# Kernel tuning notes

Hardware: AMD Instinct MI355X
Metric: run time of the kernel (lower is better)

## Reference

```python
import jax, jax.numpy as jnp
import numpy as np
from math import pi

RADIUS = 40.0  # radius_scale
B, N = 1, 512


def map_polar_sqr(x, y, eps=1e-9):
    r = jnp.sqrt(x * x + y * y + eps)
    cond1 = (x == 0.0) & (y == 0.0)
    cond2 = (jnp.abs(y) <= jnp.abs(x)) & (~cond1)
    sx = jnp.where(x == 0.0, 1.0, x)  # safe denominators
    sy = jnp.where(y == 0.0, 1.0, y)
    c = 4.0 / pi
    x2 = jnp.sign(x) * r
    y2 = c * jnp.sign(x) * r * jnp.arctan(y / sx)
    x3 = c * jnp.sign(y) * r * jnp.arctan(x / sy)
    y3 = jnp.sign(y) * r
    x_out = jnp.where(cond1, 0.0, jnp.where(cond2, x2, x3))
    y_out = jnp.where(cond1, 0.0, jnp.where(cond2, y2, y3))
    return x_out, y_out


def axis_weights(g, size):
    # F.grid_sample bilinear, align_corners=False, padding_mode='zeros':
    # pixel coord = ((g+1)*size - 1)/2; linear weights on floor/floor+1,
    # out-of-range taps drop to zero automatically (idx only covers 0..size-1).
    c = ((g + 1.0) * size - 1.0) * 0.5
    i0 = jnp.floor(c)
    f = c - i0
    idx = jnp.arange(size, dtype=g.dtype)
    m0 = (idx == i0[..., None]).astype(g.dtype)
    m1 = (idx == i0[..., None] + 1.0).astype(g.dtype)
    return (1.0 - f)[..., None] * m0 + f[..., None] * m1  # [..., size]


def cts_conv(kernel, field, center, feat, mask, radius):
    # kernel: [o, i, kD, kH, kW]; field/center: [b, n/m, 3]; feat: [b, n, i]; mask: [b, n, 1]
    rel = (field[:, None] - center[:, :, None]) / radius            # [b,m,n,3]
    r2 = jnp.sum(rel * rel, -1)                                     # [b,m,n]
    att = jax.nn.relu((1.0 - r2) ** 3)[..., None] * mask[:, None]   # [b,m,n,1]
    xs, ys = map_polar_sqr(rel[..., 0], rel[..., 1])
    zs = rel[..., 2]
    kD, kH, kW = kernel.shape[2:]
    # grid_sample coord order: grid x -> W (last dim), y -> H, z -> D (first spatial dim)
    wz = axis_weights(zs, kD)
    wy = axis_weights(ys, kH)
    wx = axis_weights(xs, kW)
    w = jnp.einsum('bmnz,bmny,bmnx->bmnzyx', wz, wy, wx)
    w = w.reshape(*w.shape[:3], -1)                                 # [b,m,n,g=kD*kH*kW]
    fa = feat[:, None] * att                                        # [b,m,n,i]
    # exact trilinear interp + neighbor contraction without the [b,m,n,o,i] tensor:
    t = jnp.einsum('bmng,bmni->bmgi', w, fa)                        # [b,m,g,i]
    K = kernel.reshape(kernel.shape[0], kernel.shape[1], -1)        # [o,i,g]
    return jnp.einsum('bmgi,oig->bmo', t, K)


def setup_inputs() -> dict:
    key = jax.random.key(0)
    ks = jax.random.split(key, 24)

    def kern(k, o, i):
        return (jax.random.uniform(k, (o, i, 4, 4, 4), dtype=jnp.float32) - 0.5) / float(np.sqrt(i))

    def lin(kw, kb, o, i):
        return (jax.random.normal(kw, (o, i), dtype=jnp.float32) * 0.05,
                jax.random.normal(kb, (o,), dtype=jnp.float32) * 0.05)

    p = jax.random.normal(ks[0], (B, N, 3), dtype=jnp.float32) * 20.0
    v = jax.random.normal(ks[1], (B, N, 3), dtype=jnp.float32)
    other_feats = jax.random.normal(ks[2], (B, N, 62), dtype=jnp.float32)
    fluid_mask = jnp.ones((B, N, 1), dtype=jnp.float32)

    k_fluid = kern(ks[3], 32, 66)
    Wf, bf = lin(ks[4], ks[5], 32, 66)
    k1 = kern(ks[6], 64, 64); W1, b1 = lin(ks[7], ks[8], 64, 64)
    k2 = kern(ks[9], 64, 64); W2, b2 = lin(ks[10], ks[11], 64, 64)
    k3 = kern(ks[12], 64, 64); W3, b3 = lin(ks[13], ks[14], 64, 64)
    k4 = kern(ks[15], 6, 64); W4, b4 = lin(ks[16], ks[17], 6, 64)
    return dict(p=p, v=v, other_feats=other_feats, fluid_mask=fluid_mask,
                k_fluid=k_fluid, Wf=Wf, bf=bf,
                k1=k1, W1=W1, b1=b1, k2=k2, W2=W2, b2=b2,
                k3=k3, W3=W3, b3=b3, k4=k4, W4=W4, b4=b4)


def reference(p, v, other_feats, fluid_mask, k_fluid, Wf, bf,
              k1, W1, b1, k2, W2, b2, k3, W3, b3, k4, W4, b4):
    feats0 = jnp.concatenate([jnp.ones_like(p[..., :1]), v, other_feats], -1)  # [b,n,66]
    oc = cts_conv(k_fluid, p, p, feats0, fluid_mask, RADIUS)
    od = feats0 @ Wf.T + bf
    output = jnp.concatenate([oc, od], -1)  # [b,n,64]
    for k, W, bb in ((k1, W1, b1), (k2, W2, b2), (k3, W3, b3), (k4, W4, b4)):
        h = jax.nn.relu(output)
        oc = cts_conv(k, p, p, h, fluid_mask, RADIUS)
        od = h @ W.T + bb
        if od.shape[-1] == output.shape[-1]:
            output = oc + od + output
        else:
            output = oc + od
    return output  # [b,n,6]
```

## Files before the change

kernel.cpp:

```cpp
#include <hip/hip_runtime.h>

typedef _Float16 f16;
typedef _Float16 f16x8 __attribute__((ext_vector_type(8)));
typedef float f32x4 __attribute__((ext_vector_type(4)));
typedef int iv2 __attribute__((ext_vector_type(2)));

#define INV_R (1.0f / 40.0f)
#define NBLK 512

#define F_BAR  0u
#define F_SELF 2304u
#define F_B0   2368u
#define F_K    2624u
#define F_HT   2286144u
#define F_T0   2695744u
#define F_T1   7119424u
#define F_T2   11379264u
#define F_T3   15639104u
#define F_T4   19898944u
#define F_OG   24158784u
#define NEED_FULL 24289856u

#define C_B0  2304u
#define C_K   2560u
#define C_HTA 2286080u
#define C_HTB 2368000u
#define C_TA  2449920u
#define C_TB  6873600u
#define C_OG  11133440u

#define K1_OFF 552960u
#define K2_OFF 1085440u
#define K3_OFF 1617920u
#define K4_OFF 2150400u

#define PREP_TOTAL 1231936

__device__ __forceinline__ void st_sys_u16(void* p, unsigned v) {
  asm volatile("global_store_short %0, %1, off sc0 sc1" :: "v"(p), "v"(v) : "memory");
}
__device__ __forceinline__ void st_sys_f32(float* p, float v) {
  asm volatile("global_store_dword %0, %1, off sc0 sc1" :: "v"(p), "v"(v) : "memory");
}
__device__ __forceinline__ void st_sys_b64(void* p, iv2 v) {
  asm volatile("global_store_dwordx2 %0, %1, off sc0 sc1" :: "v"(p), "v"(v) : "memory");
}
__device__ __forceinline__ unsigned f16bits(float x) {
  union { f16 h; unsigned short s; } cv; cv.h = (f16)x; return (unsigned)cv.s;
}

__device__ __forceinline__ unsigned bar_ld(unsigned* p) {
  return __hip_atomic_load(p, __ATOMIC_RELAXED, __HIP_MEMORY_SCOPE_AGENT);
}
__device__ void gridbar(unsigned* bar, int phase) {
  asm volatile("s_waitcnt vmcnt(0)" ::: "memory");
  __syncthreads();
  if (threadIdx.x == 0) {
    int bid = blockIdx.x;
    int cls = bid & 7;
    unsigned* xcnt = bar + cls * 32 + phase;
    unsigned* xrel = bar + 256 + cls * 32 + phase;
    unsigned* gcnt = bar + 512 + phase;
    unsigned* grel = bar + 544 + phase;
    __hip_atomic_fetch_add(xcnt, 1u, __ATOMIC_RELAXED, __HIP_MEMORY_SCOPE_AGENT);
    if (bid < 8) {
      while (bar_ld(xcnt) < (NBLK / 8)) __builtin_amdgcn_s_sleep(2);
      __hip_atomic_fetch_add(gcnt, 1u, __ATOMIC_RELAXED, __HIP_MEMORY_SCOPE_AGENT);
      if (bid == 0) {
        while (bar_ld(gcnt) < 8u) __builtin_amdgcn_s_sleep(2);
        __hip_atomic_store(grel, 1u, __ATOMIC_RELAXED, __HIP_MEMORY_SCOPE_AGENT);
      } else {
        while (bar_ld(grel) == 0u) __builtin_amdgcn_s_sleep(4);
      }
      __hip_atomic_store(xrel, 1u, __ATOMIC_RELAXED, __HIP_MEMORY_SCOPE_AGENT);
    } else {
      while (bar_ld(xrel) == 0u) __builtin_amdgcn_s_sleep(64);
    }
    asm volatile("" ::: "memory");
  }
  __syncthreads();
}

__device__ __forceinline__ float feats0_val(int ch, int n, const float* v, const float* other) {
  if (ch == 0) return 1.0f;
  if (ch < 4) return v[n * 3 + (ch - 1)];
  return other[n * 62 + (ch - 4)];
}
__device__ __forceinline__ float atan_poly(float t) {
  float t2 = t * t;
  float p = -0.0117212f;
  p = p * t2 + 0.05265332f;
  p = p * t2 - 0.11643287f;
  p = p * t2 + 0.19354346f;
  p = p * t2 - 0.33262347f;
  p = p * t2 + 0.99997726f;
  return t * p;
}
__device__ __forceinline__ void axis_w(float g, int& i0c, int& i1c, float& w0, float& w1) {
  float c = 2.0f * g + 1.5f;
  float fl = floorf(c);
  float f = c - fl;
  int i0 = (int)fl;
  w0 = (i0 >= 0 && i0 <= 3) ? (1.0f - f) : 0.0f;
  w1 = (i0 >= -1 && i0 <= 2) ? f : 0.0f;
  i0c = min(max(i0, 0), 3);
  i1c = min(max(i0 + 1, 0), 3);
}

__device__ void prep_body(const float* __restrict__ v, const float* __restrict__ other,
                          const float* __restrict__ kf, const float* __restrict__ Wf,
                          const float* __restrict__ bf,
                          const float* __restrict__ k1, const float* __restrict__ W1,
                          const float* __restrict__ k2, const float* __restrict__ W2,
                          const float* __restrict__ k3, const float* __restrict__ W3,
                          const float* __restrict__ k4, const float* __restrict__ W4,
                          f16* __restrict__ K0, float* __restrict__ B0,
                          f16* __restrict__ hT0, f16* __restrict__ t0) {
  for (int idx = blockIdx.x * 256 + threadIdx.x; idx < PREP_TOTAL; idx += NBLK * 256) {
    int e = idx;
    if (e < 40960) {
      int i = e >> 9, n = e & 511;
      float val = (i < 66) ? feats0_val(i, n, v, other) : 0.0f;
      st_sys_u16(hT0 + e, f16bits(val));
      continue;
    }
    e -= 40960;
    if (e < 49152) {
      int m = e / 96, j = e % 96;
      float val = (j < 66) ? feats0_val(j, m, v, other) : 0.0f;
      st_sys_u16(t0 + (size_t)m * 4320 + 4224 + j, f16bits(val));
      continue;
    }
    e -= 49152;
    if (e < 276480) {
      int o = e / 4320, k = e % 4320;
      float val = 0.0f;
      if (o < 32) { if (k < 4224) val = kf[o * 4224 + k]; }
      else if (k >= 4224 && k < 4290) val = Wf[(o - 32) * 66 + (k - 4224)];
      st_sys_u16(K0 + e, f16bits(val));
      continue;
    }
    e -= 276480;
    if (e < 798720) {
      int which = e / 266240, ee = e % 266240;
      const float* kk = which == 0 ? k1 : (which == 1 ? k2 : k3);
      const float* WW = which == 0 ? W1 : (which == 1 ? W2 : W3);
      int o = ee / 4160, k = ee % 4160;
      float val = (k < 4096) ? kk[o * 4096 + k] : WW[o * 64 + (k - 4096)];
      st_sys_u16(K0 + (K1_OFF / 2) + (size_t)which * 266240 + ee, f16bits(val));
      continue;
    }
    e -= 798720;
    if (e < 66560) {
      int o = e / 4160, k = e % 4160;
      float val = 0.0f;
      if (o < 6) val = (k < 4096) ? k4[o * 4096 + k] : W4[o * 64 + (k - 4096)];
      st_sys_u16(K0 + (K4_OFF / 2) + e, f16bits(val));
      continue;
    }
    e -= 66560;
    if (e < 64) st_sys_f32(&B0[e], (e < 32) ? 0.0f : bf[e - 32]);
  }
}

template<int CI, int ITILES, int KDIM>
__device__ void stage1_body(const float* __restrict__ p, const float* __restrict__ mask,
                            const f16* __restrict__ hT_in, f16* __restrict__ tout,
                            f16* __restrict__ Wl, int m, bool local) {
  const int tid = threadIdx.x;
  const int wave = tid >> 6, lane = tid & 63;
  const int row = lane & 15, kgrp = lane >> 4;
  const int grow = wave * 16 + row;

  const float pmx = p[m * 3 + 0], pmy = p[m * 3 + 1], pmz = p[m * 3 + 2];
  f32x4 acc[ITILES];
  #pragma unroll
  for (int it = 0; it < ITILES; ++it) acc[it] = f32x4{0.f, 0.f, 0.f, 0.f};

  #pragma unroll
  for (int half = 0; half < 2; ++half) {
    __syncthreads();
    int4* w4 = (int4*)Wl;
    int4 z4 = make_int4(0, 0, 0, 0);
    #pragma unroll
    for (int i = 0; i < 8; ++i) w4[tid + i * 256] = z4;
    __syncthreads();
    {
      const int n = half * 256 + tid;
      float x = (p[n * 3 + 0] - pmx) * INV_R;
      float y = (p[n * 3 + 1] - pmy) * INV_R;
      float z = (p[n * 3 + 2] - pmz) * INV_R;
      float r2 = x * x + y * y + z * z;
      float q = 1.0f - r2;
      float att = (q > 0.0f) ? q * q * q * mask[n] : 0.0f;
      bool c1 = (x == 0.0f) && (y == 0.0f);
      bool c2 = (fabsf(y) <= fabsf(x)) && !c1;
      float r = sqrtf(x * x + y * y + 1e-9f);
      float num = c2 ? y : x;
      float den = c2 ? x : y;
      float a = atan_poly(num / den);
      float s2 = copysignf(r, x), s3 = copysignf(r, y);
      const float C4PI = 1.2732395447351628f;
      float xs = c1 ? 0.0f : (c2 ? s2 : C4PI * s3 * a);
      float ys = c1 ? 0.0f : (c2 ? C4PI * s2 * a : s3);
      float zs = z;
      int iz0, iz1, iy0, iy1, ix0, ix1;
      float wz0, wz1, wy0, wy1, wx0, wx1;
      axis_w(zs, iz0, iz1, wz0, wz1);
      axis_w(ys, iy0, iy1, wy0, wy1);
      axis_w(xs, ix0, ix1, wx0, wx1);
      wz0 *= att; wz1 *= att;
      int gz[2] = {iz0 * 16, iz1 * 16};
      int gy[2] = {iy0 * 4, iy1 * 4};
      int gx[2] = {ix0, ix1};
      float wzv[2] = {wz0, wz1}, wyv[2] = {wy0, wy1}, wxv[2] = {wx0, wx1};
      #pragma unroll
      for (int za = 0; za < 2; ++za)
        #pragma unroll
        for (int ya = 0; ya < 2; ++ya)
          #pragma unroll
          for (int xa = 0; xa < 2; ++xa) {
            float w = wzv[za] * wyv[ya] * wxv[xa];
            if (w != 0.0f) {
              int g = gz[za] + gy[ya] + gx[xa];
              Wl[g * 256 + (tid ^ ((g & 7) << 3))] = (f16)w;
            }
          }
    }
    __syncthreads();
    #pragma unroll
    for (int k0 = 0; k0 < 8; ++k0) {
      const int n0l = k0 * 32 + kgrp * 8;
      f16x8 afrag = *(f16x8*)&Wl[grow * 256 + (n0l ^ ((grow & 7) << 3))];
      f16x8 bfr[ITILES];
      #pragma unroll
      for (int it = 0; it < ITILES; ++it)
        bfr[it] = *(const f16x8*)&hT_in[(it * 16 + row) * 512 + half * 256 + n0l];
      #pragma unroll
      for (int it = 0; it < ITILES; ++it)
        acc[it] = __builtin_amdgcn_mfma_f32_16x16x32_f16(afrag, bfr[it], acc[it], 0, 0, 0);
    }
  }
  const int g4 = wave * 16 + kgrp * 4;
  #pragma unroll
  for (int it = 0; it < ITILES; ++it) {
    const int icol = it * 16 + row;
    if (icol < CI) {
      union { f16 h[4]; iv2 i; short4 s; } cv;
      #pragma unroll
      for (int r = 0; r < 4; ++r) cv.h[r] = (f16)acc[it][r];
      f16* dst = &tout[(size_t)m * KDIM + icol * 64 + g4];
      if (local) *(short4*)dst = cv.s;
      else st_sys_b64(dst, cv.i);
    }
  }
}

template<int KDIM, bool RES, bool FINAL>
__device__ void stage2_body(const f16* __restrict__ t, const f16* __restrict__ Kf,
                            const float* __restrict__ bias, float* __restrict__ outG,
                            f16* __restrict__ hT_out, f16* __restrict__ tnext,
                            float* __restrict__ dout, float* __restrict__ red,
                            bool active, int mbase, int otile, bool local) {
  if (!active) return;
  constexpr int KSTEPS = KDIM / 32;
  int tid = threadIdx.x;
  int kpart = tid >> 6, lane = tid & 63;
  int row = lane & 15, kgrp = lane >> 4;
  int mrow = mbase + row;
  int ocol = otile * 16 + row;
  f32x4 acc = {0.f, 0.f, 0.f, 0.f};
  for (int ks = kpart; ks < KSTEPS; ks += 4) {
    int k0 = ks * 32 + kgrp * 8;
    f16x8 afrag = *(const f16x8*)&t[(size_t)mrow * KDIM + k0];
    f16x8 bfrag = *(const f16x8*)&Kf[(size_t)ocol * KDIM + k0];
    acc = __builtin_amdgcn_mfma_f32_16x16x32_f16(afrag, bfrag, acc, 0, 0, 0);
  }
  if (kpart > 0) {
    #pragma unroll
    for (int r = 0; r < 4; ++r)
      red[(kpart - 1) * 256 + (kgrp * 4 + r) * 16 + row] = acc[r];
  }
  __syncthreads();
  if (kpart == 0) {
    #pragma unroll
    for (int kw = 0; kw < 3; ++kw)
      #pragma unroll
      for (int r = 0; r < 4; ++r)
        acc[r] += red[kw * 256 + (kgrp * 4 + r) * 16 + row];
    #pragma unroll
    for (int r = 0; r < 4; ++r) {
      int mm = mbase + kgrp * 4 + r;
      int oo = ocol;
      if (FINAL) {
        if (oo < 6) dout[mm * 6 + oo] = acc[r] + bias[oo];
      } else {
        float val = acc[r] + bias[oo];
        if (RES) val += outG[mm * 64 + oo];
        outG[mm * 64 + oo] = val;
        float h = fmaxf(val, 0.0f);
        unsigned hb = f16bits(h);
        st_sys_u16(&hT_out[oo * 512 + mm], hb);
        f16* tp = &tnext[(size_t)mm * 4160 + 4096 + oo];
        if (local) { union { unsigned short u; f16 f; } c; c.u = (unsigned short)hb; *tp = c.f; }
        else st_sys_u16(tp, hb);
      }
    }
  }
}

__global__ __launch_bounds__(256, 2) void mega_kernel(
    const float* p, const float* v, const float* other, const float* mask,
    const float* kf, const float* Wf, const float* bf,
    const float* k1, const float* W1, const float* b1,
    const float* k2, const float* W2, const float* b2,
    const float* k3, const float* W3, const float* b3,
    const float* k4, const float* W4, const float* b4,
    float* dout, char* ws) {
  __shared__ int4 blob[4096];
  __shared__ unsigned s_rank;
  f16* Wl = (f16*)blob;
  float* red = (float*)blob;
  unsigned* bar = (unsigned*)(ws + F_BAR);
  unsigned* selfcnt = (unsigned*)(ws + F_SELF);
  unsigned* ovp = selfcnt + 8;

  unsigned xcc;
  asm volatile("s_getreg_b32 %0, hwreg(20, 0, 32)" : "=s"(xcc));
  xcc &= 7u;
  if (threadIdx.x == 0) {
    unsigned r = atomicAdd(&selfcnt[xcc], 1u);
    if (r >= 64u) __hip_atomic_store(ovp, 1u, __ATOMIC_RELAXED, __HIP_MEMORY_SCOPE_AGENT);
    s_rank = r;
  }
  __syncthreads();
  unsigned rank = s_rank;

  f16* K0  = (f16*)(ws + F_K);
  float* B0 = (float*)(ws + F_B0);
  f16* hT0 = (f16*)(ws + F_HT);
  f16* hT1 = hT0 + 40960;
  f16* hT2 = hT0 + 81920;
  f16* hT3 = hT0 + 122880;
  f16* hT4 = hT0 + 163840;
  f16* t0 = (f16*)(ws + F_T0);
  f16* t1 = (f16*)(ws + F_T1);
  f16* t2 = (f16*)(ws + F_T2);
  f16* t3 = (f16*)(ws + F_T3);
  f16* t4 = (f16*)(ws + F_T4);
  float* outG = (float*)(ws + F_OG);

  prep_body(v, other, kf, Wf, bf, k1, W1, k2, W2, k3, W3, k4, W4, K0, B0, hT0, t0);
  gridbar(bar, 0);

  bool local = (__hip_atomic_load(ovp, __ATOMIC_RELAXED, __HIP_MEMORY_SCOPE_AGENT) == 0u);
  int m1    = local ? (int)(xcc * 64u + rank) : (int)blockIdx.x;
  bool s2a  = local ? (rank < 16u) : (blockIdx.x < 128);
  int tix   = local ? (int)rank : (int)blockIdx.x;
  int ot    = tix & 3;
  int mbase = local ? (int)(xcc * 64u + (rank >> 2) * 16u) : ((int)(blockIdx.x >> 2) * 16);

  stage1_body<66, 5, 4320>(p, mask, hT0, t0, Wl, m1, local);
  gridbar(bar, 1);
  stage2_body<4320, false, false>(t0, K0, B0, outG, hT1, t1, nullptr, red, s2a, mbase, ot, local);
  gridbar(bar, 2);
  stage1_body<64, 4, 4160>(p, mask, hT1, t1, Wl, m1, local);
  gridbar(bar, 3);
  stage2_body<4160, true, false>(t1, K0 + K1_OFF / 2, b1, outG, hT2, t2, nullptr, red, s2a, mbase, ot, local);
  gridbar(bar, 4);
  stage1_body<64, 4, 4160>(p, mask, hT2, t2, Wl, m1, local);
  gridbar(bar, 5);
  stage2_body<4160, true, false>(t2, K0 + K2_OFF / 2, b2, outG, hT3, t3, nullptr, red, s2a, mbase, ot, local);
  gridbar(bar, 6);
  stage1_body<64, 4, 4160>(p, mask, hT3, t3, Wl, m1, local);
  gridbar(bar, 7);
  stage2_body<4160, true, false>(t3, K0 + K3_OFF / 2, b3, outG, hT4, t4, nullptr, red, s2a, mbase, ot, local);
  gridbar(bar, 8);
  stage1_body<64, 4, 4160>(p, mask, hT4, t4, Wl, m1, local);
  gridbar(bar, 9);
  stage2_body<4160, false, true>(t4, K0 + K4_OFF / 2, b4, outG, nullptr, nullptr, dout, red, s2a, mbase, ot, local);
}

__global__ __launch_bounds__(256) void prep_g(
    const float* v, const float* other, const float* kf, const float* Wf, const float* bf,
    const float* k1, const float* W1, const float* k2, const float* W2,
    const float* k3, const float* W3, const float* k4, const float* W4,
    f16* K0, float* B0, f16* hT0, f16* t0) {
  prep_body(v, other, kf, Wf, bf, k1, W1, k2, W2, k3, W3, k4, W4, K0, B0, hT0, t0);
}
template<int CI, int ITILES, int KDIM>
__global__ __launch_bounds__(256) void stage1_g(const float* p, const float* mask,
                                                const f16* hT_in, f16* tout) {
  __shared__ int4 blob[2048];
  stage1_body<CI, ITILES, KDIM>(p, mask, hT_in, tout, (f16*)blob, blockIdx.x, false);
}
template<int KDIM, bool RES, bool FINAL>
__global__ __launch_bounds__(256) void stage2_g(const f16* t, const f16* Kf,
                                                const float* bias, float* outG,
                                                f16* hT_out, f16* tnext, float* dout) {
  __shared__ float red[3 * 256];
  stage2_body<KDIM, RES, FINAL>(t, Kf, bias, outG, hT_out, tnext, dout, red,
                                blockIdx.x < 128, ((int)blockIdx.x >> 2) * 16,
                                (int)blockIdx.x & 3, false);
}

extern "C" void kernel_launch(void* const* d_in, const int* in_sizes, int n_in,
                              void* d_out, int out_size, void* d_ws, size_t ws_size,
                              hipStream_t stream) {
  const float* p     = (const float*)d_in[0];
  const float* v     = (const float*)d_in[1];
  const float* other = (const float*)d_in[2];
  const float* mask  = (const float*)d_in[3];
  const float* kf    = (const float*)d_in[4];
  const float* Wf    = (const float*)d_in[5];
  const float* bf    = (const float*)d_in[6];
  const float* k1    = (const float*)d_in[7];
  const float* W1    = (const float*)d_in[8];
  const float* b1    = (const float*)d_in[9];
  const float* k2    = (const float*)d_in[10];
  const float* W2    = (const float*)d_in[11];
  const float* b2    = (const float*)d_in[12];
  const float* k3    = (const float*)d_in[13];
  const float* W3    = (const float*)d_in[14];
  const float* b3    = (const float*)d_in[15];
  const float* k4    = (const float*)d_in[16];
  const float* W4    = (const float*)d_in[17];
  const float* b4    = (const float*)d_in[18];
  float* dout = (float*)d_out;
  char* ws = (char*)d_ws;
  (void)in_sizes; (void)n_in; (void)out_size;

  int maxb = 0;
  hipError_t e1 = hipOccupancyMaxActiveBlocksPerMultiprocessor(
      &maxb, (const void*)mega_kernel, 256, 0);
  if (e1 == hipSuccess && maxb >= 2 && ws_size >= NEED_FULL) {
    hipMemsetAsync(ws, 0, 2368, stream);
    void* args[] = {
      (void*)&p, (void*)&v, (void*)&other, (void*)&mask,
      (void*)&kf, (void*)&Wf, (void*)&bf,
      (void*)&k1, (void*)&W1, (void*)&b1,
      (void*)&k2, (void*)&W2, (void*)&b2,
      (void*)&k3, (void*)&W3, (void*)&b3,
      (void*)&k4, (void*)&W4, (void*)&b4,
      (void*)&dout, (void*)&ws
    };
    hipError_t e2 = hipLaunchCooperativeKernel((const void*)mega_kernel, dim3(NBLK),
                                               dim3(256), args, 0, stream);
    if (e2 == hipSuccess) return;
  }

  f16* K0  = (f16*)(ws + C_K);
  float* B0 = (float*)(ws + C_B0);
  f16* hTA = (f16*)(ws + C_HTA);
  f16* hTB = (f16*)(ws + C_HTB);
  f16* tA  = (f16*)(ws + C_TA);
  f16* tB  = (f16*)(ws + C_TB);
  float* outG = (float*)(ws + C_OG);

  prep_g<<<NBLK, 256, 0, stream>>>(v, other, kf, Wf, bf, k1, W1, k2, W2, k3, W3, k4, W4,
                                   K0, B0, hTA, tA);
  stage1_g<66, 5, 4320><<<NBLK, 256, 0, stream>>>(p, mask, hTA, tA);
  stage2_g<4320, false, false><<<128, 256, 0, stream>>>(tA, K0, B0, outG, hTB, tB, nullptr);
  stage1_g<64, 4, 4160><<<NBLK, 256, 0, stream>>>(p, mask, hTB, tB);
  stage2_g<4160, true, false><<<128, 256, 0, stream>>>(tB, K0 + K1_OFF / 2, b1, outG, hTA, tA, nullptr);
  stage1_g<64, 4, 4160><<<NBLK, 256, 0, stream>>>(p, mask, hTA, tA);
  stage2_g<4160, true, false><<<128, 256, 0, stream>>>(tA, K0 + K2_OFF / 2, b2, outG, hTB, tB, nullptr);
  stage1_g<64, 4, 4160><<<NBLK, 256, 0, stream>>>(p, mask, hTB, tB);
  stage2_g<4160, true, false><<<128, 256, 0, stream>>>(tB, K0 + K3_OFF / 2, b3, outG, hTA, tA, nullptr);
  stage1_g<64, 4, 4160><<<NBLK, 256, 0, stream>>>(p, mask, hTA, tA);
  stage2_g<4160, false, true><<<128, 256, 0, stream>>>(tA, K0 + K4_OFF / 2, b4, outG, nullptr, nullptr, dout);
}
```

Baseline: 190.5 us.

## Replicate converted kernel weights per XCC for local reads and unroll stage2

When blocks are placed locally and the workspace is large enough, each XCC's 64 blocks now write their own private fp16 copy of all conv/linear weights with plain stores instead of system-scope stores. Stage2 then reads weights from its XCC's copy, so reads stay within that XCC's L2 rather than crossing XCCs. The weight conversion moves after an extra grid barrier, so each XCC does the full conversion redundantly, and stage2's k-loop gets an unroll-4 pragma. This adds roughly 16 MB of workspace, one more grid barrier, and more conversion work per block.

Result: no change. 190.6 us (+0.0%).

```diff
diff --git a/kernel.cpp b/kernel.cpp
--- a/kernel.cpp
+++ b/kernel.cpp
@@ -20,6 +20,11 @@
 #define F_T4   19898944u
 #define F_OG   24158784u
 #define NEED_FULL 24289856u
+#define F_KP   24289856u
+#define NEED_KTPRIV 40274496u
+
+#define KT_ELEMS 1141760u
+#define KT_BYTES 2283520u
 
 #define C_B0  2304u
 #define C_K   2560u
@@ -33,8 +38,6 @@
 #define K2_OFF 1085440u
 #define K3_OFF 1617920u
 #define K4_OFF 2150400u
-
-#define PREP_TOTAL 1231936
 
 __device__ __forceinline__ void st_sys_u16(void* p, unsigned v) {
   asm volatile("global_store_short %0, %1, off sc0 sc1" :: "v"(p), "v"(v) : "memory");
@@ -107,16 +110,11 @@
   i1c = min(max(i0 + 1, 0), 3);
 }
 
-__device__ void prep_body(const float* __restrict__ v, const float* __restrict__ other,
-                          const float* __restrict__ kf, const float* __restrict__ Wf,
-                          const float* __restrict__ bf,
-                          const float* __restrict__ k1, const float* __restrict__ W1,
-                          const float* __restrict__ k2, const float* __restrict__ W2,
-                          const float* __restrict__ k3, const float* __restrict__ W3,
-                          const float* __restrict__ k4, const float* __restrict__ W4,
-                          f16* __restrict__ K0, float* __restrict__ B0,
-                          f16* __restrict__ hT0, f16* __restrict__ t0) {
-  for (int idx = blockIdx.x * 256 + threadIdx.x; idx < PREP_TOTAL; idx += NBLK * 256) {
+__device__ void prep_shared(const float* __restrict__ v, const float* __restrict__ other,
+                            const float* __restrict__ bf,
+                            float* __restrict__ B0, f16* __restrict__ hT0,
+                            f16* __restrict__ t0) {
+  for (int idx = blockIdx.x * 256 + threadIdx.x; idx < 90176; idx += NBLK * 256) {
     int e = idx;
     if (e < 40960) {
       int i = e >> 9, n = e & 511;
@@ -132,34 +130,38 @@
       continue;
     }
     e -= 49152;
-    if (e < 276480) {
-      int o = e / 4320, k = e % 4320;
-      float val = 0.0f;
+    if (e < 64) st_sys_f32(&B0[e], (e < 32) ? 0.0f : bf[e - 32]);
+  }
+}
+
+template<bool SYS>
+__device__ void prep_kt(const float* __restrict__ kf, const float* __restrict__ Wf,
+                        const float* __restrict__ k1, const float* __restrict__ W1,
+                        const float* __restrict__ k2, const float* __restrict__ W2,
+                        const float* __restrict__ k3, const float* __restrict__ W3,
+                        const float* __restrict__ k4, const float* __restrict__ W4,
+                        f16* __restrict__ dst, unsigned start, unsigned stride) {
+  for (unsigned e = start; e < KT_ELEMS; e += stride) {
+    unsigned ee = e;
+    float val = 0.0f;
+    if (ee < 276480u) {
+      int o = ee / 4320, k = ee % 4320;
       if (o < 32) { if (k < 4224) val = kf[o * 4224 + k]; }
       else if (k >= 4224 && k < 4290) val = Wf[(o - 32) * 66 + (k - 4224)];
-      st_sys_u16(K0 + e, f16bits(val));
-      continue;
-    }
-    e -= 276480;
-    if (e < 798720) {
-      int which = e / 266240, ee = e % 266240;
+    } else if (ee < 1075200u) {
+      unsigned f = ee - 276480u;
+      int which = f / 266240, g = f % 266240;
       const float* kk = which == 0 ? k1 : (which == 1 ? k2 : k3);
       const float* WW = which == 0 ? W1 : (which == 1 ? W2 : W3);
-      int o = ee / 4160, k = ee % 4160;
-      float val = (k < 4096) ? kk[o * 4096 + k] : WW[o * 64 + (k - 4096)];
-      st_sys_u16(K0 + (K1_OFF / 2) + (size_t)which * 266240 + ee, f16bits(val));
-      continue;
-    }
-    e -= 798720;
-    if (e < 66560) {
-      int o = e / 4160, k = e % 4160;
-      float val = 0.0f;
+      int o = g / 4160, k = g % 4160;
+      val = (k < 4096) ? kk[o * 4096 + k] : WW[o * 64 + (k - 4096)];
+    } else {
+      unsigned g = ee - 1075200u;
+      int o = g / 4160, k = g % 4160;
       if (o < 6) val = (k < 4096) ? k4[o * 4096 + k] : W4[o * 64 + (k - 4096)];
-      st_sys_u16(K0 + (K4_OFF / 2) + e, f16bits(val));
-      continue;
-    }
-    e -= 66560;
-    if (e < 64) st_sys_f32(&B0[e], (e < 32) ? 0.0f : bf[e - 32]);
+    }
+    if (SYS) st_sys_u16(dst + e, f16bits(val));
+    else dst[e] = (f16)val;
   }
 }
 
@@ -270,6 +272,7 @@
   int mrow = mbase + row;
   int ocol = otile * 16 + row;
   f32x4 acc = {0.f, 0.f, 0.f, 0.f};
+  #pragma unroll 4
   for (int ks = kpart; ks < KSTEPS; ks += 4) {
     int k0 = ks * 32 + kgrp * 8;
     f16x8 afrag = *(const f16x8*)&t[(size_t)mrow * KDIM + k0];
@@ -316,7 +319,7 @@
     const float* k2, const float* W2, const float* b2,
     const float* k3, const float* W3, const float* b3,
     const float* k4, const float* W4, const float* b4,
-    float* dout, char* ws) {
+    float* dout, char* ws, int ktpriv) {
   __shared__ int4 blob[4096];
   __shared__ unsigned s_rank;
   f16* Wl = (f16*)blob;
@@ -336,7 +339,6 @@
   __syncthreads();
   unsigned rank = s_rank;
 
-  f16* K0  = (f16*)(ws + F_K);
   float* B0 = (float*)(ws + F_B0);
   f16* hT0 = (f16*)(ws + F_HT);
   f16* hT1 = hT0 + 40960;
@@ -350,10 +352,24 @@
   f16* t4 = (f16*)(ws + F_T4);
   float* outG = (float*)(ws + F_OG);
 
-  prep_body(v, other, kf, Wf, bf, k1, W1, k2, W2, k3, W3, k4, W4, K0, B0, hT0, t0);
   gridbar(bar, 0);
-
   bool local = (__hip_atomic_load(ovp, __ATOMIC_RELAXED, __HIP_MEMORY_SCOPE_AGENT) == 0u);
+  bool kpriv = local && (ktpriv != 0);
+
+  f16* Kb;
+  if (kpriv && xcc > 0) Kb = (f16*)(ws + F_KP + (size_t)(xcc - 1) * KT_BYTES);
+  else Kb = (f16*)(ws + F_K);
+
+  prep_shared(v, other, bf, B0, hT0, t0);
+  if (kpriv) {
+    prep_kt<false>(kf, Wf, k1, W1, k2, W2, k3, W3, k4, W4, Kb,
+                   rank * 256u + threadIdx.x, 64u * 256u);
+  } else {
+    prep_kt<true>(kf, Wf, k1, W1, k2, W2, k3, W3, k4, W4, (f16*)(ws + F_K),
+                  blockIdx.x * 256u + threadIdx.x, NBLK * 256u);
+  }
+  gridbar(bar, 1);
+
   int m1    = local ? (int)(xcc * 64u + rank) : (int)blockIdx.x;
   bool s2a  = local ? (rank < 16u) : (blockIdx.x < 128);
   int tix   = local ? (int)rank : (int)blockIdx.x;
@@ -361,24 +377,24 @@
   int mbase = local ? (int)(xcc * 64u + (rank >> 2) * 16u) : ((int)(blockIdx.x >> 2) * 16);
 
   stage1_body<66, 5, 4320>(p, mask, hT0, t0, Wl, m1, local);
-  gridbar(bar, 1);
-  stage2_body<4320, false, false>(t0, K0, B0, outG, hT1, t1, nullptr, red, s2a, mbase, ot, local);
   gridbar(bar, 2);
+  stage2_body<4320, false, false>(t0, Kb, B0, outG, hT1, t1, nullptr, red, s2a, mbase, ot, local);
+  gridbar(bar, 3);
   stage1_body<64, 4, 4160>(p, mask, hT1, t1, Wl, m1, local);
-  gridbar(bar, 3);
-  stage2_body<4160, true, false>(t1, K0 + K1_OFF / 2, b1, outG, hT2, t2, nullptr, red, s2a, mbase, ot, local);
   gridbar(bar, 4);
+  stage2_body<4160, true, false>(t1, Kb + K1_OFF / 2, b1, outG, hT2, t2, nullptr, red, s2a, mbase, ot, local);
+  gridbar(bar, 5);
   stage1_body<64, 4, 4160>(p, mask, hT2, t2, Wl, m1, local);
-  gridbar(bar, 5);
-  stage2_body<4160, true, false>(t2, K0 + K2_OFF / 2, b2, outG, hT3, t3, nullptr, red, s2a, mbase, ot, local);
   gridbar(bar, 6);
+  stage2_body<4160, true, false>(t2, Kb + K2_OFF / 2, b2, outG, hT3, t3, nullptr, red, s2a, mbase, ot, local);
+  gridbar(bar, 7);
   stage1_body<64, 4, 4160>(p, mask, hT3, t3, Wl, m1, local);
-  gridbar(bar, 7);
-  stage2_body<4160, true, false>(t3, K0 + K3_OFF / 2, b3, outG, hT4, t4, nullptr, red, s2a, mbase, ot, local);
   gridbar(bar, 8);
+  stage2_body<4160, true, false>(t3, Kb + K3_OFF / 2, b3, outG, hT4, t4, nullptr, red, s2a, mbase, ot, local);
+  gridbar(bar, 9);
   stage1_body<64, 4, 4160>(p, mask, hT4, t4, Wl, m1, local);
-  gridbar(bar, 9);
-  stage2_body<4160, false, true>(t4, K0 + K4_OFF / 2, b4, outG, nullptr, nullptr, dout, red, s2a, mbase, ot, local);
+  gridbar(bar, 10);
+  stage2_body<4160, false, true>(t4, Kb + K4_OFF / 2, b4, outG, nullptr, nullptr, dout, red, s2a, mbase, ot, local);
 }
 
 __global__ __launch_bounds__(256) void prep_g(
@@ -386,7 +402,9 @@
     const float* k1, const float* W1, const float* k2, const float* W2,
     const float* k3, const float* W3, const float* k4, const float* W4,
     f16* K0, float* B0, f16* hT0, f16* t0) {
-  prep_body(v, other, kf, Wf, bf, k1, W1, k2, W2, k3, W3, k4, W4, K0, B0, hT0, t0);
+  prep_shared(v, other, bf, B0, hT0, t0);
+  prep_kt<false>(kf, Wf, k1, W1, k2, W2, k3, W3, k4, W4, K0,
+                 blockIdx.x * 256u + threadIdx.x, NBLK * 256u);
 }
 template<int CI, int ITILES, int KDIM>
 __global__ __launch_bounds__(256) void stage1_g(const float* p, const float* mask,
@@ -434,6 +452,7 @@
   hipError_t e1 = hipOccupancyMaxActiveBlocksPerMultiprocessor(
       &maxb, (const void*)mega_kernel, 256, 0);
   if (e1 == hipSuccess && maxb >= 2 && ws_size >= NEED_FULL) {
+    int ktpriv = (ws_size >= NEED_KTPRIV) ? 1 : 0;
     hipMemsetAsync(ws, 0, 2368, stream);
     void* args[] = {
       (void*)&p, (void*)&v, (void*)&other, (void*)&mask,
@@ -442,7 +461,7 @@
       (void*)&k2, (void*)&W2, (void*)&b2,
       (void*)&k3, (void*)&W3, (void*)&b3,
       (void*)&k4, (void*)&W4, (void*)&b4,
-      (void*)&dout, (void*)&ws
+      (void*)&dout, (void*)&ws, (void*)&ktpriv
     };
     hipError_t e2 = hipLaunchCooperativeKernel((const void*)mega_kernel, dim3(NBLK),
                                                dim3(256), args, 0, stream);
```
